# Optimization experiments

Hardware: AMD Instinct MI355X
Metric: run time of the kernel (lower is better)

## Reference

```python
import jax, jax.numpy as jnp
import numpy as np

B, N, C = 16, 4096, 64
EPS = 1e-12  # F.normalize default eps


def setup_inputs() -> dict:
    key = jax.random.key(0)
    x = jax.random.normal(key, (B, N, C), dtype=jnp.float32)
    return {"x": x}


def _sop_forward(x):
    # x: [B, N, C]  (tupleLen == 1 in the standard forward path)
    b, n, c = x.shape
    # per-point outer products, max-pooled over points: [B, C, C]
    outer = x[:, :, :, None] * x[:, :, None, :]          # [B, N, C, C]
    pooled = jnp.max(outer, axis=1)                      # [B, C, C]
    # power-normalization via batched SVD with alpha = 0.5
    # (torch.svd returns V; u @ diag(s^0.5) @ v^T == u @ diag(s^0.5) @ vh)
    u, s, vh = jnp.linalg.svd(pooled, full_matrices=False)
    pooled = jnp.einsum('bij,bj,bjk->bik', u, jnp.sqrt(s), vh)  # [B, C, C]
    # vectorize (is_vec=True) and L2-normalize along last dim
    v = pooled.reshape(b, c * c)                         # [B, C*C]
    norm = jnp.maximum(jnp.linalg.norm(v, axis=-1, keepdims=True), EPS)
    return v / norm                                      # squeeze([B,1,C*C]) -> [B, C*C]


def reference(x):
    return _sop_forward(x)
```

## Files before the change

### kernel.cpp

```cpp
#include <hip/hip_runtime.h>
#include <math.h>

#define NSWEEP 6
#define NR (NSWEEP * 63)

typedef __attribute__((ext_vector_type(2))) float f32x2;

__global__ __launch_bounds__(256) void pool_kernel(const float* __restrict__ x,
                                                   float* __restrict__ part,
                                                   int G) {
  __shared__ float xs[4096];
  const int t = threadIdx.x;
  const int blk = blockIdx.x;
  const int b = blk / G, g = blk % G;
  const int npb = 4096 / G;
  const int ntile = npb >> 6;
  const int n0 = g * npb;
  const int i0 = (t >> 4) * 4;
  const int j0 = (t & 15) * 4;

  float mv[4][4];
#pragma unroll
  for (int a = 0; a < 4; ++a)
#pragma unroll
    for (int c = 0; c < 4; ++c) mv[a][c] = -INFINITY;

  const float4* src = reinterpret_cast<const float4*>(x + ((size_t)b * 4096 + n0) * 64);
  float4* xs4 = reinterpret_cast<float4*>(xs);

  for (int tile = 0; tile < ntile; ++tile) {
#pragma unroll
    for (int q = 0; q < 4; ++q) xs4[t + 256 * q] = src[(size_t)tile * 1024 + t + 256 * q];
    __syncthreads();
#pragma unroll 4
    for (int n = 0; n < 64; ++n) {
      const float4 vi = *reinterpret_cast<const float4*>(&xs[n * 64 + i0]);
      const float4 vj = *reinterpret_cast<const float4*>(&xs[n * 64 + j0]);
      const float fi[4] = {vi.x, vi.y, vi.z, vi.w};
      const float fj[4] = {vj.x, vj.y, vj.z, vj.w};
#pragma unroll
      for (int a = 0; a < 4; ++a)
#pragma unroll
        for (int c = 0; c < 4; ++c)
          mv[a][c] = fmaxf(mv[a][c], fi[a] * fj[c]);
    }
    __syncthreads();
  }

#pragma unroll
  for (int a = 0; a < 4; ++a)
#pragma unroll
    for (int c = 0; c < 4; ++c)
      xs[(i0 + a) * 64 + (j0 + c)] = mv[a][c];
  __syncthreads();

  float* dst = part + ((size_t)b * G + g) * 4096;
#pragma unroll
  for (int q = 0; q < 16; ++q) dst[t + 256 * q] = xs[t + 256 * q];
}

__device__ __forceinline__ float bperm(int byteaddr, float v) {
  return __int_as_float(__builtin_amdgcn_ds_bpermute(byteaddr, __float_as_int(v)));
}

__global__ __launch_bounds__(256, 1) void svd_kernel(const float* __restrict__ part,
                                                     float* __restrict__ out, int G) {
  __shared__ __align__(16) float Al[64 * 68];
  __shared__ __align__(16) float Vl[64 * 68];
  __shared__ float2 ring[64][64];
  __shared__ float red[4];
  __shared__ int pflag_s, cflag_s;

  const int b = blockIdx.x;
  const int t = threadIdx.x;
  const int wave = t >> 6, lane = t & 63;
  const int lane4 = lane << 2;

  if (t == 0) { pflag_s = 0; cflag_s = 0; }

  const float4* p4 = reinterpret_cast<const float4*>(part) + (size_t)b * G * 1024;
  float4 acc[4];
#pragma unroll
  for (int u = 0; u < 4; ++u) acc[u] = p4[t + 256 * u];
#pragma unroll 2
  for (int g = 1; g < G; ++g) {
#pragma unroll
    for (int u = 0; u < 4; ++u) {
      const float4 v = p4[(size_t)g * 1024 + t + 256 * u];
      acc[u].x = fmaxf(acc[u].x, v.x);
      acc[u].y = fmaxf(acc[u].y, v.y);
      acc[u].z = fmaxf(acc[u].z, v.z);
      acc[u].w = fmaxf(acc[u].w, v.w);
    }
  }
#pragma unroll
  for (int u = 0; u < 4; ++u) {
    const int idx = t + 256 * u;
    const int i = idx >> 4;
    const int j = (idx & 15) * 4;
    *reinterpret_cast<float4*>(&Al[i * 68 + j]) = acc[u];
  }
  __syncthreads();

  if (wave == 0) {
    f32x2 g2[32], ex2[32];
#pragma unroll
    for (int k = 0; k < 32; ++k)
      g2[k] = (f32x2){Al[(2 * k) * 68 + lane], Al[(2 * k + 1) * 68 + lane]};

    float a;
    {
      f32x2 n0 = (f32x2)(0.0f), n1 = (f32x2)(0.0f), n2 = (f32x2)(0.0f), n3 = (f32x2)(0.0f);
#pragma unroll
      for (int k = 0; k < 32; k += 4) {
        n0 = g2[k] * g2[k] + n0;
        n1 = g2[k + 1] * g2[k + 1] + n1;
        n2 = g2[k + 2] * g2[k + 2] + n2;
        n3 = g2[k + 3] * g2[k + 3] + n3;
      }
      const f32x2 nt = (n0 + n1) + (n2 + n3);
      a = nt.x + nt.y;
    }

    int m = 1;
    int addr = lane4 ^ (m << 2);
#pragma unroll
    for (int k = 0; k < 32; ++k) {
      ex2[k].x = bperm(addr, g2[k].x);
      ex2[k].y = bperm(addr, g2[k].y);
    }
    float bb = bperm(addr, a);

#pragma unroll 1
    for (int rg = 0; rg < NR; ++rg) {
      float d;
      {
        f32x2 d0 = (f32x2)(0.0f), d1 = (f32x2)(0.0f), d2 = (f32x2)(0.0f), d3 = (f32x2)(0.0f);
        f32x2 d4 = (f32x2)(0.0f), d5 = (f32x2)(0.0f), d6 = (f32x2)(0.0f), d7 = (f32x2)(0.0f);
#pragma unroll
        for (int k = 0; k < 32; k += 8) {
          d0 = g2[k] * ex2[k] + d0;
          d1 = g2[k + 1] * ex2[k + 1] + d1;
          d2 = g2[k + 2] * ex2[k + 2] + d2;
          d3 = g2[k + 3] * ex2[k + 3] + d3;
          d4 = g2[k + 4] * ex2[k + 4] + d4;
          d5 = g2[k + 5] * ex2[k + 5] + d5;
          d6 = g2[k + 6] * ex2[k + 6] + d6;
          d7 = g2[k + 7] * ex2[k + 7] + d7;
        }
        const f32x2 dt = ((d0 + d1) + (d2 + d3)) + ((d4 + d5) + (d6 + d7));
        d = dt.x + dt.y;
      }

      const int partner = lane ^ m;
      const float u = (bb - a) * 0.5f;
      const float sg = (u != 0.0f) ? copysignf(1.0f, u)
                                   : ((lane < partner) ? 1.0f : -1.0f);
      const float q = fmaf(u, u, d * d);
      float c, s;
      if (q > 0.0f) {
        const float rh = rsqrtf(q);
        const float cc = fmaf(0.5f * fabsf(u), rh, 0.5f);
        const float rc = rsqrtf(cc);
        c = cc * rc;
        s = d * sg * rh * 0.5f * rc;
      } else {
        c = 1.0f; s = 0.0f;
      }
      const float ns = -s;
      const float aupd = fmaf(c * c, a, fmaf(s * s, bb, -2.0f * (c * s) * d));

      ring[rg & 63][lane] = make_float2(c, s);
      if ((rg & 15) == 15) {
        if (lane == 0)
          __hip_atomic_store(&pflag_s, rg + 1, __ATOMIC_RELEASE, __HIP_MEMORY_SCOPE_WORKGROUP);
        int cd = __hip_atomic_load(&cflag_s, __ATOMIC_ACQUIRE, __HIP_MEMORY_SCOPE_WORKGROUP);
        while (rg + 1 - cd > 40) {
          __builtin_amdgcn_s_sleep(1);
          cd = __hip_atomic_load(&cflag_s, __ATOMIC_ACQUIRE, __HIP_MEMORY_SCOPE_WORKGROUP);
        }
      }

      const int mn = (m == 63) ? 1 : m + 1;
      const int addrn = lane4 ^ (mn << 2);

      float bbn = bperm(addrn, aupd);

      const f32x2 c2 = {c, c}, ns2 = {ns, ns};
#pragma unroll
      for (int k = 0; k < 32; ++k) {
        g2[k] = ns2 * ex2[k] + c2 * g2[k];
        ex2[k].x = bperm(addrn, g2[k].x);
        ex2[k].y = bperm(addrn, g2[k].y);
      }

      if (mn == 1) {
        f32x2 n0 = (f32x2)(0.0f), n1 = (f32x2)(0.0f), n2 = (f32x2)(0.0f), n3 = (f32x2)(0.0f);
#pragma unroll
        for (int k = 0; k < 32; k += 4) {
          n0 = g2[k] * g2[k] + n0;
          n1 = g2[k + 1] * g2[k + 1] + n1;
          n2 = g2[k + 2] * g2[k + 2] + n2;
          n3 = g2[k + 3] * g2[k + 3] + n3;
        }
        const f32x2 nt = (n0 + n1) + (n2 + n3);
        a = nt.x + nt.y;
        bbn = bperm(addrn, a);
      } else {
        a = aupd;
      }
      bb = bbn;
      m = mn;
    }
    if (lane == 0)
      __hip_atomic_store(&pflag_s, NR, __ATOMIC_RELEASE, __HIP_MEMORY_SCOPE_WORKGROUP);

    float s2;
    {
      f32x2 n0 = (f32x2)(0.0f), n1 = (f32x2)(0.0f), n2 = (f32x2)(0.0f), n3 = (f32x2)(0.0f);
#pragma unroll
      for (int k = 0; k < 32; k += 4) {
        n0 = g2[k] * g2[k] + n0;
        n1 = g2[k + 1] * g2[k + 1] + n1;
        n2 = g2[k + 2] * g2[k + 2] + n2;
        n3 = g2[k + 3] * g2[k + 3] + n3;
      }
      const f32x2 nt = (n0 + n1) + (n2 + n3);
      s2 = nt.x + nt.y;
    }
    const float sigma = sqrtf(s2);
    const float coef = (sigma > 1e-30f) ? rsqrtf(sigma) : 0.0f;
#pragma unroll
    for (int k = 0; k < 32; ++k) {
      Al[(2 * k) * 68 + lane] = g2[k].x * coef;
      Al[(2 * k + 1) * 68 + lane] = g2[k].y * coef;
    }

  } else if (wave == 1) {
    f32x2 v2[32];
#pragma unroll
    for (int k = 0; k < 32; ++k)
      v2[k] = (f32x2){(2 * k == lane) ? 1.0f : 0.0f, (2 * k + 1 == lane) ? 1.0f : 0.0f};

    int m = 1;
    int addr = lane4 ^ (m << 2);
    int seen = 0;
#pragma unroll 1
    for (int rg = 0; rg < NR; ++rg) {
      if (seen < rg + 1) {
        for (;;) {
          seen = __hip_atomic_load(&pflag_s, __ATOMIC_ACQUIRE, __HIP_MEMORY_SCOPE_WORKGROUP);
          if (seen >= rg + 1) break;
          __builtin_amdgcn_s_sleep(1);
        }
      }
      const float2 cs = ring[rg & 63][lane];
      const float c = cs.x, ns = -cs.y;
      const f32x2 c2 = {c, c}, ns2 = {ns, ns};

#pragma unroll
      for (int k = 0; k < 32; ++k) {
        f32x2 e;
        e.x = bperm(addr, v2[k].x);
        e.y = bperm(addr, v2[k].y);
        v2[k] = ns2 * e + c2 * v2[k];
      }
      m = (m == 63) ? 1 : m + 1;
      addr = lane4 ^ (m << 2);

      if ((rg & 15) == 15 && lane == 0)
        __hip_atomic_store(&cflag_s, rg + 1, __ATOMIC_RELEASE, __HIP_MEMORY_SCOPE_WORKGROUP);
    }
#pragma unroll
    for (int k = 0; k < 32; ++k) {
      Vl[(2 * k) * 68 + lane] = v2[k].x;
      Vl[(2 * k + 1) * 68 + lane] = v2[k].y;
    }
  }
  __syncthreads();

  float wr[64];
#pragma unroll
  for (int jb = 0; jb < 16; ++jb) {
    const float4 v4 = *reinterpret_cast<const float4*>(&Al[lane * 68 + jb * 4]);
    wr[4 * jb] = v4.x; wr[4 * jb + 1] = v4.y; wr[4 * jb + 2] = v4.z; wr[4 * jb + 3] = v4.w;
  }
  __syncthreads();

  const int j0 = wave * 16;
  float rvals[16];
  float ssq = 0.0f;
#pragma unroll 4
  for (int jj = 0; jj < 16; ++jj) {
    const float4* vr = reinterpret_cast<const float4*>(&Vl[(j0 + jj) * 68]);
    float c0 = 0, c1 = 0, c2 = 0, c3 = 0;
#pragma unroll
    for (int kb = 0; kb < 16; ++kb) {
      const float4 vv = vr[kb];
      c0 = fmaf(wr[4 * kb], vv.x, c0);
      c1 = fmaf(wr[4 * kb + 1], vv.y, c1);
      c2 = fmaf(wr[4 * kb + 2], vv.z, c2);
      c3 = fmaf(wr[4 * kb + 3], vv.w, c3);
    }
    const float accv = (c0 + c1) + (c2 + c3);
    rvals[jj] = accv;
    ssq = fmaf(accv, accv, ssq);
  }
#pragma unroll
  for (int jj = 0; jj < 4; ++jj)
    *reinterpret_cast<float4*>(&Al[lane * 68 + j0 + 4 * jj]) =
        make_float4(rvals[4 * jj], rvals[4 * jj + 1], rvals[4 * jj + 2], rvals[4 * jj + 3]);

#pragma unroll
  for (int off = 32; off; off >>= 1) ssq += __shfl_xor(ssq, off, 64);
  if (lane == 0) red[wave] = ssq;
  __syncthreads();
  const float rn = rsqrtf(fmaxf(red[0] + red[1] + red[2] + red[3], 1e-24f));

#pragma unroll
  for (int u = 0; u < 16; ++u) {
    const int e = t + 256 * u;
    out[(size_t)b * 4096 + e] = Al[(e >> 6) * 68 + (e & 63)] * rn;
  }
}

extern "C" void kernel_launch(void* const* d_in, const int* in_sizes, int n_in,
                              void* d_out, int out_size, void* d_ws, size_t ws_size,
                              hipStream_t stream) {
  const float* x = (const float*)d_in[0];
  float* out = (float*)d_out;
  float* part = (float*)d_ws;

  int G = 32;
  while (G > 1 && (size_t)16 * G * 4096 * 4 > ws_size) G >>= 1;

  pool_kernel<<<dim3(16 * G), dim3(256), 0, stream>>>(x, part, G);
  svd_kernel<<<dim3(16), dim3(256), 0, stream>>>(part, out, G);
}
```

Baseline: 269.7 us.

## Merge V rotation into the Jacobi wave, dropping the producer-consumer ring

The V-matrix rotation updates move out of a second wave, which consumed rotation coefficients through an LDS ring with atomic flags and sleep polling. Wave 0 now applies each rotation to both G and V in registers. This removes the LDS ring traffic, the flag handshakes and the sleep-based waiting. In exchange it roughly doubles the per-sweep serial work on one wave, adds 64 more registers, and gives up the two-wave overlap.

```diff
diff --git a/kernel.cpp b/kernel.cpp
--- a/kernel.cpp
+++ b/kernel.cpp
@@ -67,16 +67,12 @@
                                                      float* __restrict__ out, int G) {
   __shared__ __align__(16) float Al[64 * 68];
   __shared__ __align__(16) float Vl[64 * 68];
-  __shared__ float2 ring[64][64];
   __shared__ float red[4];
-  __shared__ int pflag_s, cflag_s;
 
   const int b = blockIdx.x;
   const int t = threadIdx.x;
   const int wave = t >> 6, lane = t & 63;
   const int lane4 = lane << 2;
-
-  if (t == 0) { pflag_s = 0; cflag_s = 0; }
 
   const float4* p4 = reinterpret_cast<const float4*>(part) + (size_t)b * G * 1024;
   float4 acc[4];
@@ -103,10 +99,12 @@
   __syncthreads();
 
   if (wave == 0) {
-    f32x2 g2[32], ex2[32];
-#pragma unroll
-    for (int k = 0; k < 32; ++k)
+    f32x2 g2[32], ex2[32], v2[32];
+#pragma unroll
+    for (int k = 0; k < 32; ++k) {
       g2[k] = (f32x2){Al[(2 * k) * 68 + lane], Al[(2 * k + 1) * 68 + lane]};
+      v2[k] = (f32x2){(2 * k == lane) ? 1.0f : 0.0f, (2 * k + 1 == lane) ? 1.0f : 0.0f};
+    }
 
     float a;
     {
@@ -169,29 +167,26 @@
       }
       const float ns = -s;
       const float aupd = fmaf(c * c, a, fmaf(s * s, bb, -2.0f * (c * s) * d));
-
-      ring[rg & 63][lane] = make_float2(c, s);
-      if ((rg & 15) == 15) {
-        if (lane == 0)
-          __hip_atomic_store(&pflag_s, rg + 1, __ATOMIC_RELEASE, __HIP_MEMORY_SCOPE_WORKGROUP);
-        int cd = __hip_atomic_load(&cflag_s, __ATOMIC_ACQUIRE, __HIP_MEMORY_SCOPE_WORKGROUP);
-        while (rg + 1 - cd > 40) {
-          __builtin_amdgcn_s_sleep(1);
-          cd = __hip_atomic_load(&cflag_s, __ATOMIC_ACQUIRE, __HIP_MEMORY_SCOPE_WORKGROUP);
-        }
-      }
+      const f32x2 c2 = {c, c}, ns2 = {ns, ns};
 
       const int mn = (m == 63) ? 1 : m + 1;
       const int addrn = lane4 ^ (mn << 2);
 
       float bbn = bperm(addrn, aupd);
 
-      const f32x2 c2 = {c, c}, ns2 = {ns, ns};
 #pragma unroll
       for (int k = 0; k < 32; ++k) {
         g2[k] = ns2 * ex2[k] + c2 * g2[k];
         ex2[k].x = bperm(addrn, g2[k].x);
         ex2[k].y = bperm(addrn, g2[k].y);
+      }
+
+#pragma unroll
+      for (int k = 0; k < 32; ++k) {
+        f32x2 e;
+        e.x = bperm(addr, v2[k].x);
+        e.y = bperm(addr, v2[k].y);
+        v2[k] = ns2 * e + c2 * v2[k];
       }
 
       if (mn == 1) {
@@ -211,9 +206,8 @@
       }
       bb = bbn;
       m = mn;
-    }
-    if (lane == 0)
-      __hip_atomic_store(&pflag_s, NR, __ATOMIC_RELEASE, __HIP_MEMORY_SCOPE_WORKGROUP);
+      addr = addrn;
+    }
 
     float s2;
     {
@@ -234,45 +228,6 @@
     for (int k = 0; k < 32; ++k) {
       Al[(2 * k) * 68 + lane] = g2[k].x * coef;
       Al[(2 * k + 1) * 68 + lane] = g2[k].y * coef;
-    }
-
-  } else if (wave == 1) {
-    f32x2 v2[32];
-#pragma unroll
-    for (int k = 0; k < 32; ++k)
-      v2[k] = (f32x2){(2 * k == lane) ? 1.0f : 0.0f, (2 * k + 1 == lane) ? 1.0f : 0.0f};
-
-    int m = 1;
-    int addr = lane4 ^ (m << 2);
-    int seen = 0;
-#pragma unroll 1
-    for (int rg = 0; rg < NR; ++rg) {
-      if (seen < rg + 1) {
-        for (;;) {
-          seen = __hip_atomic_load(&pflag_s, __ATOMIC_ACQUIRE, __HIP_MEMORY_SCOPE_WORKGROUP);
-          if (seen >= rg + 1) break;
-          __builtin_amdgcn_s_sleep(1);
-        }
-      }
-      const float2 cs = ring[rg & 63][lane];
-      const float c = cs.x, ns = -cs.y;
-      const f32x2 c2 = {c, c}, ns2 = {ns, ns};
-
-#pragma unroll
-      for (int k = 0; k < 32; ++k) {
-        f32x2 e;
-        e.x = bperm(addr, v2[k].x);
-        e.y = bperm(addr, v2[k].y);
-        v2[k] = ns2 * e + c2 * v2[k];
-      }
-      m = (m == 63) ? 1 : m + 1;
-      addr = lane4 ^ (m << 2);
-
-      if ((rg & 15) == 15 && lane == 0)
-        __hip_atomic_store(&cflag_s, rg + 1, __ATOMIC_RELEASE, __HIP_MEMORY_SCOPE_WORKGROUP);
-    }
-#pragma unroll
-    for (int k = 0; k < 32; ++k) {
       Vl[(2 * k) * 68 + lane] = v2[k].x;
       Vl[(2 * k + 1) * 68 + lane] = v2[k].y;
     }
```

Result: slower. 408.2 us (+51.4%).
